# Kernel tuning notes

Hardware: AMD Instinct MI355X
Metric: run time of the kernel (lower is better)

## Reference

```python
import jax, jax.numpy as jnp
import numpy as np

MODEL_DIM = 1024
N_HEADS = 16
HEAD_DIM = 64  # q_dim == k_dim == v_dim


def setup_inputs() -> dict:
    key = jax.random.key(0)
    ks = jax.random.split(key, 7)
    B, S = 4, 2048
    scale = 1.0 / np.sqrt(MODEL_DIM)
    return {
        "q": jax.random.normal(ks[0], (B, S, MODEL_DIM), dtype=jnp.float32),
        "k": jax.random.normal(ks[1], (B, S, MODEL_DIM), dtype=jnp.float32),
        "v": jax.random.normal(ks[2], (B, S, MODEL_DIM), dtype=jnp.float32),
        # Linear weights stored as [out, in] like torch; no biases.
        "wq": jax.random.normal(ks[3], (N_HEADS * HEAD_DIM, MODEL_DIM), dtype=jnp.float32) * scale,
        "wk": jax.random.normal(ks[4], (N_HEADS * HEAD_DIM, MODEL_DIM), dtype=jnp.float32) * scale,
        "wv": jax.random.normal(ks[5], (N_HEADS * HEAD_DIM, MODEL_DIM), dtype=jnp.float32) * scale,
        "wo": jax.random.normal(ks[6], (MODEL_DIM, N_HEADS * HEAD_DIM), dtype=jnp.float32) * scale,
    }


def reference(q, k, v, wq, wk, wv, wo):
    B, Sq, _ = q.shape
    Sk = k.shape[1]
    # projections: [B,S,D] @ W^T -> [B,S,H*dh] -> [B,H,S,dh]
    qh = (q @ wq.T).reshape(B, Sq, N_HEADS, HEAD_DIM).transpose(0, 2, 1, 3)
    kh = (k @ wk.T).reshape(B, Sk, N_HEADS, HEAD_DIM).transpose(0, 2, 1, 3)
    vh = (v @ wv.T).reshape(B, Sk, N_HEADS, HEAD_DIM).transpose(0, 2, 1, 3)
    # scores [B,H,Sq,Sk], scaled by sqrt(k_dim)
    scores = jnp.einsum('bhqd,bhkd->bhqk', qh, kh) / jnp.sqrt(jnp.float32(HEAD_DIM))
    attn = jax.nn.softmax(scores, axis=-1)
    ctx = jnp.einsum('bhqk,bhkd->bhqd', attn, vh)  # [B,H,Sq,dh]
    ctx = ctx.transpose(0, 2, 1, 3).reshape(B, Sq, N_HEADS * HEAD_DIM)
    return ctx @ wo.T
```

## Files before the change

### kernel.cpp

```cpp
#include <hip/hip_runtime.h>
#include <cstdint>
#include <cstddef>


typedef _Float16 f16x8 __attribute__((ext_vector_type(8)));
typedef _Float16 f16x4 __attribute__((ext_vector_type(4)));
typedef _Float16 f16x2 __attribute__((ext_vector_type(2)));
typedef __fp16 h16x2 __attribute__((ext_vector_type(2)));
typedef float f32x4 __attribute__((ext_vector_type(4)));
typedef float f32x16 __attribute__((ext_vector_type(16)));
typedef unsigned u32x4 __attribute__((ext_vector_type(4)));
typedef int i32x2 __attribute__((ext_vector_type(2)));

#define LDS_CAST(p) ((__attribute__((address_space(3))) void*)(p))
#define GLB_CAST(p) ((const __attribute__((address_space(1))) void*)(p))

__device__ __forceinline__ void gload_lds16(const void* g, void* l) {
  __builtin_amdgcn_global_load_lds(GLB_CAST(g), LDS_CAST(l), 16, 0, 0);
}

__device__ __forceinline__ float fexp2(float x) {
#if __has_builtin(__builtin_amdgcn_exp2f)
  return __builtin_amdgcn_exp2f(x);
#else
  return exp2f(x);
#endif
}

__device__ __forceinline__ f16x2 pkrtz(float a, float b) {
  h16x2 r = __builtin_amdgcn_cvt_pkrtz(a, b);
  return __builtin_bit_cast(f16x2, r);
}

__device__ __forceinline__ float dot2acc(f16x2 a, float acc) {
#if __has_builtin(__builtin_amdgcn_fdot2)
  const f16x2 one2 = {(_Float16)1.0f, (_Float16)1.0f};
  return __builtin_amdgcn_fdot2(a, one2, acc, false);
#else
  return acc + (float)a[0] + (float)a[1];
#endif
}

__device__ __forceinline__ void pl32swap(unsigned& a, unsigned& b) {
#if __has_builtin(__builtin_amdgcn_permlane32_swap)
  i32x2 r = __builtin_amdgcn_permlane32_swap((int)a, (int)b, false, false);
  a = (unsigned)r[0];
  b = (unsigned)r[1];
#else
  asm("v_permlane32_swap_b32 %0, %1" : "+v"(a), "+v"(b));
#endif
}

__global__ void cvt_all(const float* __restrict__ q, const float* __restrict__ k,
                        const float* __restrict__ v, const float* __restrict__ wq,
                        const float* __restrict__ wk, const float* __restrict__ wv,
                        const float* __restrict__ wo, _Float16* __restrict__ oq,
                        _Float16* __restrict__ ok, _Float16* __restrict__ ov,
                        _Float16* __restrict__ owq, _Float16* __restrict__ owk,
                        _Float16* __restrict__ owv, _Float16* __restrict__ owo) {
  int id = blockIdx.x;
  const float* in;
  _Float16* out;
  int base;
  if (id < 24576) {
    int z = id >> 13;
    base = (id & 8191) * 256;
    in = z == 0 ? q : z == 1 ? k : v;
    out = z == 0 ? oq : z == 1 ? ok : ov;
  } else {
    int id2 = id - 24576;
    int z = id2 >> 10;
    base = (id2 & 1023) * 256;
    in = z == 0 ? wq : z == 1 ? wk : z == 2 ? wv : wo;
    out = z == 0 ? owq : z == 1 ? owk : z == 2 ? owv : owo;
  }
  int i = base + threadIdx.x;
  float4 vv = ((const float4*)in)[i];
  f16x4 o = {(_Float16)vv.x, (_Float16)vv.y, (_Float16)vv.z, (_Float16)vv.w};
  ((f16x4*)out)[i] = o;
}

template <int MODE>
__device__ __forceinline__ void gemm_core(const _Float16* __restrict__ A,
                                          const _Float16* __restrict__ W,
                                          void* __restrict__ C, float scale,
                                          _Float16* As, _Float16* Bs) {
  constexpr int K = 1024, N = 1024;
  const int tid = threadIdx.x;
  const int wid = tid >> 6;
  const int lane = tid & 63;
  const int quad = lane >> 4;
  const int l16 = lane & 15;
  const int wm = wid >> 1;
  const int wn = wid & 1;

  int lin = blockIdx.y * 8 + blockIdx.x;
  int swz = (lin & 7) * 64 + (lin >> 3);
  const int m0 = (swz >> 3) * 128;
  const int n0 = (swz & 7) * 128;

  const _Float16* Ag = A + (size_t)m0 * K;
  const _Float16* Bg = W + (size_t)n0 * K;

  f32x4 acc[4][4];
#pragma unroll
  for (int i = 0; i < 4; i++)
#pragma unroll
    for (int j = 0; j < 4; j++) acc[i][j] = (f32x4){0.f, 0.f, 0.f, 0.f};

  const int lrow = lane >> 2;
  const int swsrc = ((lane & 3) ^ ((lane >> 3) & 3)) * 8;

  auto stage = [&](_Float16* Ad, _Float16* Bd, int k0) {
#pragma unroll
    for (int i = 0; i < 2; i++) {
      int issue = wid * 2 + i;
      gload_lds16(Ag + (size_t)(issue * 16 + lrow) * K + k0 + swsrc,
                  Ad + issue * 512);
      gload_lds16(Bg + (size_t)(issue * 16 + lrow) * K + k0 + swsrc,
                  Bd + issue * 512);
    }
  };

  const int swq = (quad ^ ((l16 >> 1) & 3)) * 8;

  auto compute = [&](const _Float16* Ab, const _Float16* Bb) {
    f16x8 af[4], bfr[4];
#pragma unroll
    for (int mt = 0; mt < 4; mt++)
      af[mt] = *(const f16x8*)&Ab[(wm * 64 + mt * 16 + l16) * 32 + swq];
#pragma unroll
    for (int nt = 0; nt < 4; nt++)
      bfr[nt] = *(const f16x8*)&Bb[(wn * 64 + nt * 16 + l16) * 32 + swq];
#pragma unroll
    for (int mt = 0; mt < 4; mt++)
#pragma unroll
      for (int nt = 0; nt < 4; nt++)
        acc[mt][nt] = __builtin_amdgcn_mfma_f32_16x16x32_f16(
            af[mt], bfr[nt], acc[mt][nt], 0, 0, 0);
  };

  _Float16* A0 = As;
  _Float16* A1 = As + 4096;
  _Float16* B0 = Bs;
  _Float16* B1 = Bs + 4096;

  stage(A0, B0, 0);
  asm volatile("s_waitcnt vmcnt(0)" ::: "memory");
  __builtin_amdgcn_s_barrier();

  for (int g = 0; g < 15; g++) {
    int t2 = g * 2;
    stage(A1, B1, (t2 + 1) * 32);
    compute(A0, B0);
    asm volatile("s_waitcnt vmcnt(0)" ::: "memory");
    __builtin_amdgcn_s_barrier();
    stage(A0, B0, (t2 + 2) * 32);
    compute(A1, B1);
    asm volatile("s_waitcnt vmcnt(0)" ::: "memory");
    __builtin_amdgcn_s_barrier();
  }
  stage(A1, B1, 31 * 32);
  compute(A0, B0);
  asm volatile("s_waitcnt vmcnt(0)" ::: "memory");
  __builtin_amdgcn_s_barrier();
  compute(A1, B1);

#pragma unroll
  for (int mt = 0; mt < 4; mt++) {
#pragma unroll
    for (int nt = 0; nt < 4; nt++) {
#pragma unroll
      for (int r = 0; r < 4; r++) {
        int m = m0 + wm * 64 + mt * 16 + quad * 4 + r;
        int n = n0 + wn * 64 + nt * 16 + l16;
        float v = acc[mt][nt][r] * scale;
        if (MODE == 0) {
          ((float*)C)[(size_t)m * N + n] = v;
        } else {
          int b = m >> 11, s = m & 2047;
          int h = n >> 6, dd = n & 63;
          size_t bh = (size_t)(b * 16 + h);
          if (MODE == 1) {
            ((_Float16*)C)[(bh * 2048 + s) * 64 + dd] = (_Float16)v;
          } else if (MODE == 3) {
            int kt2 = s >> 5, l32k = s & 31;
            int s4 = dd >> 4, hi8 = (dd >> 3) & 1, j = dd & 7;
            size_t idx = (bh * 32 + (kt2 >> 1)) * 8192 +
                         (((kt2 & 1) * 4 + s4) * 512) + (hi8 * 32 + l32k) * 8 +
                         j;
            ((_Float16*)C)[idx] = (_Float16)v;
          } else {
            int kt = s >> 6, ks = (s >> 4) & 3, hi8 = (s >> 3) & 1, j = s & 7;
            int dt = dd >> 5, l32v = dd & 31;
            size_t idx = (bh * 32 + kt) * 8192 + 4096 + ((dt * 4 + ks) * 512) +
                         (hi8 * 32 + l32v) * 8 + j;
            ((_Float16*)C)[idx] = (_Float16)v;
          }
        }
      }
    }
  }
}

__global__ __launch_bounds__(256, 4) void gemm_qkv(
    const _Float16* __restrict__ qb, const _Float16* __restrict__ kb,
    const _Float16* __restrict__ vb, const _Float16* __restrict__ wq,
    const _Float16* __restrict__ wk, const _Float16* __restrict__ wv,
    _Float16* __restrict__ Qh, _Float16* __restrict__ KVf) {
  __shared__ _Float16 As[2 * 128 * 32];
  __shared__ _Float16 Bs[2 * 128 * 32];
  if (blockIdx.z == 0)
    gemm_core<1>(qb, wq, Qh, 0.18033688f, As, Bs);
  else if (blockIdx.z == 1)
    gemm_core<3>(kb, wk, KVf, 1.0f, As, Bs);
  else
    gemm_core<4>(vb, wv, KVf, 1.0f, As, Bs);
}

__global__ __launch_bounds__(256, 4) void gemm_wo(
    const _Float16* __restrict__ ctx, const _Float16* __restrict__ wo,
    float* __restrict__ out) {
  __shared__ _Float16 As[2 * 128 * 32];
  __shared__ _Float16 Bs[2 * 128 * 32];
  gemm_core<0>(ctx, wo, out, 1.0f, As, Bs);
}

__global__ __launch_bounds__(256, 3) void attn_kernel(
    const _Float16* __restrict__ Qh, const _Float16* __restrict__ KVf,
    _Float16* __restrict__ ctx) {
  __shared__ _Float16 sKV[3][8192];

  const int id = blockIdx.x;
  const int xcd = id & 7;
  const int sub = id >> 3;
  const int bh = xcd * 8 + (sub >> 4);
  const int qt = sub & 15;
  const int tid = threadIdx.x;
  const int wid = tid >> 6;
  const int lane = tid & 63;
  const int l32 = lane & 31;
  const int hi = lane >> 5;

  const _Float16* Qg = Qh + ((size_t)bh * 2048 + qt * 128 + wid * 32) * 64;
  const _Float16* KVb = KVf + (size_t)bh * 262144;

  f16x8 aq[4];
#pragma unroll
  for (int s = 0; s < 4; s++)
    aq[s] = *(const f16x8*)(Qg + (size_t)l32 * 64 + s * 16 + hi * 8);

  f32x16 acc[2];
#pragma unroll
  for (int i = 0; i < 16; i++) {
    acc[0][i] = 0.f;
    acc[1][i] = 0.f;
  }
  float lsA = 0.f, lsB = 0.f;

  auto stage = [&](int buf, int kt) {
    const _Float16* t = KVb + (size_t)kt * 8192;
#pragma unroll
    for (int i = 0; i < 4; i++) {
      int c = wid * 4 + i;
      gload_lds16(t + c * 512 + lane * 8, &sKV[buf][c * 512]);
    }
  };

  auto body = [&](const _Float16* Ks) {
    const _Float16* Vs = Ks + 4096;
#pragma unroll
    for (int st = 0; st < 2; st++) {
      f16x8 kf[4];
#pragma unroll
      for (int s = 0; s < 4; s++)
        kf[s] = *(const f16x8*)&Ks[(st * 4 + s) * 512 + lane * 8];

      f32x16 sacc;
#pragma unroll
      for (int i = 0; i < 16; i++) sacc[i] = 0.f;
#pragma unroll
      for (int s = 0; s < 4; s++)
        sacc =
            __builtin_amdgcn_mfma_f32_32x32x16_f16(kf[s], aq[s], sacc, 0, 0, 0);

      f16x8 vta[2], vtb[2];
#pragma unroll
      for (int kh = 0; kh < 2; kh++) {
        int g = st * 2 + kh;
        vta[kh] = *(const f16x8*)&Vs[g * 512 + lane * 8];
        vtb[kh] = *(const f16x8*)&Vs[(4 + g) * 512 + lane * 8];
      }

      unsigned hw[8];
#pragma unroll
      for (int i = 0; i < 8; i++) {
        f16x2 hh = pkrtz(fexp2(sacc[2 * i]), fexp2(sacc[2 * i + 1]));
        if (i & 1)
          lsB = dot2acc(hh, lsB);
        else
          lsA = dot2acc(hh, lsA);
        hw[i] = __builtin_bit_cast(unsigned, hh);
      }

#pragma unroll
      for (int kh = 0; kh < 2; kh++) {
        unsigned w0 = hw[4 * kh + 0], w2 = hw[4 * kh + 2];
        unsigned w1 = hw[4 * kh + 1], w3 = hw[4 * kh + 3];
        pl32swap(w0, w2);
        pl32swap(w1, w3);
        u32x4 wv4 = {w0, w1, w2, w3};
        f16x8 pfrag = __builtin_bit_cast(f16x8, wv4);
        acc[0] = __builtin_amdgcn_mfma_f32_32x32x16_f16(vta[kh], pfrag, acc[0],
                                                        0, 0, 0);
        acc[1] = __builtin_amdgcn_mfma_f32_32x32x16_f16(vtb[kh], pfrag, acc[1],
                                                        0, 0, 0);
      }
    }
  };

  stage(0, 0);
  for (int g = 0; g < 10; g++) {
    int t3 = g * 3;
    stage(1, t3 + 1);
    asm volatile("s_waitcnt vmcnt(4)" ::: "memory");
    __builtin_amdgcn_s_barrier();
    asm volatile("" ::: "memory");
    body(sKV[0]);
    stage(2, t3 + 2);
    asm volatile("s_waitcnt vmcnt(4)" ::: "memory");
    __builtin_amdgcn_s_barrier();
    asm volatile("" ::: "memory");
    body(sKV[1]);
    stage(0, t3 + 3);
    asm volatile("s_waitcnt vmcnt(4)" ::: "memory");
    __builtin_amdgcn_s_barrier();
    asm volatile("" ::: "memory");
    body(sKV[2]);
  }
  stage(1, 31);
  asm volatile("s_waitcnt vmcnt(4)" ::: "memory");
  __builtin_amdgcn_s_barrier();
  asm volatile("" ::: "memory");
  body(sKV[0]);
  asm volatile("s_waitcnt vmcnt(0)" ::: "memory");
  __builtin_amdgcn_s_barrier();
  asm volatile("" ::: "memory");
  body(sKV[1]);

  float lsum = lsA + lsB;
  float l = lsum + __shfl_xor(lsum, 32);
  float inv = 1.f / l;
  const int b = bh >> 4, h = bh & 15;
  int q = qt * 128 + wid * 32 + l32;
  _Float16* outp = ctx + ((size_t)b * 2048 + q) * 1024 + h * 64;
#pragma unroll
  for (int dt = 0; dt < 2; dt++)
#pragma unroll
    for (int g = 0; g < 4; g++) {
      f16x4 o;
#pragma unroll
      for (int c = 0; c < 4; c++) o[c] = (_Float16)(acc[dt][g * 4 + c] * inv);
      *(f16x4*)(outp + dt * 32 + g * 8 + hi * 4) = o;
    }
}

extern "C" void kernel_launch(void* const* d_in, const int* in_sizes, int n_in,
                              void* d_out, int out_size, void* d_ws,
                              size_t ws_size, hipStream_t stream) {
  const float* q = (const float*)d_in[0];
  const float* k = (const float*)d_in[1];
  const float* v = (const float*)d_in[2];
  const float* wq = (const float*)d_in[3];
  const float* wk = (const float*)d_in[4];
  const float* wv = (const float*)d_in[5];
  const float* wo = (const float*)d_in[6];
  float* out = (float*)d_out;

  const size_t SD = (size_t)8192 * 1024;
  const size_t WSZ = (size_t)1024 * 1024;

  _Float16* ws = (_Float16*)d_ws;
  _Float16* qb = ws;
  _Float16* kb = ws + 1 * SD;
  _Float16* vb = ws + 2 * SD;
  _Float16* Qh = ws + 3 * SD;
  _Float16* KVf = ws + 4 * SD;
  _Float16* ctx = ws + 6 * SD;
  _Float16* wqb = ws + 7 * SD;
  _Float16* wkb = wqb + WSZ;
  _Float16* wvb = wqb + 2 * WSZ;
  _Float16* wob = wqb + 3 * WSZ;

  cvt_all<<<dim3(28672), 256, 0, stream>>>(q, k, v, wq, wk, wv, wo, qb, kb, vb,
                                           wqb, wkb, wvb, wob);

  gemm_qkv<<<dim3(8, 64, 3), 256, 0, stream>>>(qb, kb, vb, wqb, wkb, wvb, Qh,
                                               KVf);

  attn_kernel<<<dim3(1024), 256, 0, stream>>>(Qh, KVf, ctx);

  gemm_wo<<<dim3(8, 64), 256, 0, stream>>>(ctx, wob, out);
}
```

Baseline: 332.4 us.

## Fuse fp32-to-fp16 activation conversion into QKV projection GEMM loads

Removes the separate pass that converts q, k and v from fp32 to fp16. The QKV GEMM now stages fp32 activation tiles straight into LDS with an XOR swizzle and converts them to fp16 when forming MFMA fragments. Only the weights are still converted in a small pre-kernel. This saves a full read-write round trip over about 100MB of activations. In exchange the A tile uses twice the LDS, occupancy bounds drop from 4 to 3 blocks, the per-tile global reads double, and conversion instructions are added to the inner loop, where each A element is converted once per N-tile.

```diff
diff --git a/kernel.cpp b/kernel.cpp
--- a/kernel.cpp
+++ b/kernel.cpp
@@ -51,40 +51,25 @@
 #endif
 }
 
-__global__ void cvt_all(const float* __restrict__ q, const float* __restrict__ k,
-                        const float* __restrict__ v, const float* __restrict__ wq,
-                        const float* __restrict__ wk, const float* __restrict__ wv,
-                        const float* __restrict__ wo, _Float16* __restrict__ oq,
-                        _Float16* __restrict__ ok, _Float16* __restrict__ ov,
-                        _Float16* __restrict__ owq, _Float16* __restrict__ owk,
-                        _Float16* __restrict__ owv, _Float16* __restrict__ owo) {
+__global__ void cvt_w(const float* __restrict__ wq, const float* __restrict__ wk,
+                      const float* __restrict__ wv, const float* __restrict__ wo,
+                      _Float16* __restrict__ owq, _Float16* __restrict__ owk,
+                      _Float16* __restrict__ owv, _Float16* __restrict__ owo) {
   int id = blockIdx.x;
-  const float* in;
-  _Float16* out;
-  int base;
-  if (id < 24576) {
-    int z = id >> 13;
-    base = (id & 8191) * 256;
-    in = z == 0 ? q : z == 1 ? k : v;
-    out = z == 0 ? oq : z == 1 ? ok : ov;
-  } else {
-    int id2 = id - 24576;
-    int z = id2 >> 10;
-    base = (id2 & 1023) * 256;
-    in = z == 0 ? wq : z == 1 ? wk : z == 2 ? wv : wo;
-    out = z == 0 ? owq : z == 1 ? owk : z == 2 ? owv : owo;
-  }
-  int i = base + threadIdx.x;
-  float4 vv = ((const float4*)in)[i];
-  f16x4 o = {(_Float16)vv.x, (_Float16)vv.y, (_Float16)vv.z, (_Float16)vv.w};
+  int z = id >> 10;
+  const float* in = z == 0 ? wq : z == 1 ? wk : z == 2 ? wv : wo;
+  _Float16* out = z == 0 ? owq : z == 1 ? owk : z == 2 ? owv : owo;
+  int i = (id & 1023) * 256 + threadIdx.x;
+  float4 v = ((const float4*)in)[i];
+  f16x4 o = {(_Float16)v.x, (_Float16)v.y, (_Float16)v.z, (_Float16)v.w};
   ((f16x4*)out)[i] = o;
 }
 
-template <int MODE>
-__device__ __forceinline__ void gemm_core(const _Float16* __restrict__ A,
+template <int MODE, bool AF32>
+__device__ __forceinline__ void gemm_core(const void* __restrict__ Aptr,
                                           const _Float16* __restrict__ W,
                                           void* __restrict__ C, float scale,
-                                          _Float16* As, _Float16* Bs) {
+                                          void* AsRaw, _Float16* Bs) {
   constexpr int K = 1024, N = 1024;
   const int tid = threadIdx.x;
   const int wid = tid >> 6;
@@ -99,8 +84,11 @@
   const int m0 = (swz >> 3) * 128;
   const int n0 = (swz & 7) * 128;
 
-  const _Float16* Ag = A + (size_t)m0 * K;
+  const float* Ag32 = (const float*)Aptr + (size_t)m0 * K;
+  const _Float16* Ag16 = (const _Float16*)Aptr + (size_t)m0 * K;
   const _Float16* Bg = W + (size_t)n0 * K;
+  float* As32 = (float*)AsRaw;
+  _Float16* As16 = (_Float16*)AsRaw;
 
   f32x4 acc[4][4];
 #pragma unroll
@@ -111,24 +99,57 @@
   const int lrow = lane >> 2;
   const int swsrc = ((lane & 3) ^ ((lane >> 3) & 3)) * 8;
 
-  auto stage = [&](_Float16* Ad, _Float16* Bd, int k0) {
+  auto stageAB16 = [&](_Float16* Ad, _Float16* Bd, int k0) {
 #pragma unroll
     for (int i = 0; i < 2; i++) {
       int issue = wid * 2 + i;
-      gload_lds16(Ag + (size_t)(issue * 16 + lrow) * K + k0 + swsrc,
+      gload_lds16(Ag16 + (size_t)(issue * 16 + lrow) * K + k0 + swsrc,
                   Ad + issue * 512);
       gload_lds16(Bg + (size_t)(issue * 16 + lrow) * K + k0 + swsrc,
                   Bd + issue * 512);
     }
   };
+  auto stageB = [&](_Float16* Bd, int k0) {
+#pragma unroll
+    for (int i = 0; i < 2; i++) {
+      int issue = wid * 2 + i;
+      gload_lds16(Bg + (size_t)(issue * 16 + lrow) * K + k0 + swsrc,
+                  Bd + issue * 512);
+    }
+  };
+  const int a32row = lane >> 3;
+  const int a32sl = ((lane & 7) ^ (lane >> 3)) * 4;
+  auto stageA32 = [&](float* Ad, int k0) {
+#pragma unroll
+    for (int i = 0; i < 4; i++) {
+      int c = wid * 4 + i;
+      gload_lds16(Ag32 + (size_t)(c * 8 + a32row) * K + k0 + a32sl,
+                  Ad + c * 256);
+    }
+  };
 
   const int swq = (quad ^ ((l16 >> 1) & 3)) * 8;
-
-  auto compute = [&](const _Float16* Ab, const _Float16* Bb) {
+  const int ax = l16 & 7;
+
+  auto compute = [&](const void* Ab, const _Float16* Bb) {
     f16x8 af[4], bfr[4];
-#pragma unroll
-    for (int mt = 0; mt < 4; mt++)
-      af[mt] = *(const f16x8*)&Ab[(wm * 64 + mt * 16 + l16) * 32 + swq];
+    if constexpr (AF32) {
+      const float* A32 = (const float*)Ab;
+#pragma unroll
+      for (int mt = 0; mt < 4; mt++) {
+        int row = wm * 64 + mt * 16 + l16;
+        f32x4 a0 = *(const f32x4*)&A32[row * 32 + (((2 * quad) ^ ax) * 4)];
+        f32x4 a1 = *(const f32x4*)&A32[row * 32 + (((2 * quad + 1) ^ ax) * 4)];
+        af[mt] = (f16x8){(_Float16)a0[0], (_Float16)a0[1], (_Float16)a0[2],
+                         (_Float16)a0[3], (_Float16)a1[0], (_Float16)a1[1],
+                         (_Float16)a1[2], (_Float16)a1[3]};
+      }
+    } else {
+      const _Float16* A16 = (const _Float16*)Ab;
+#pragma unroll
+      for (int mt = 0; mt < 4; mt++)
+        af[mt] = *(const f16x8*)&A16[(wm * 64 + mt * 16 + l16) * 32 + swq];
+    }
 #pragma unroll
     for (int nt = 0; nt < 4; nt++)
       bfr[nt] = *(const f16x8*)&Bb[(wn * 64 + nt * 16 + l16) * 32 + swq];
@@ -140,31 +161,58 @@
             af[mt], bfr[nt], acc[mt][nt], 0, 0, 0);
   };
 
-  _Float16* A0 = As;
-  _Float16* A1 = As + 4096;
   _Float16* B0 = Bs;
   _Float16* B1 = Bs + 4096;
 
-  stage(A0, B0, 0);
-  asm volatile("s_waitcnt vmcnt(0)" ::: "memory");
-  __builtin_amdgcn_s_barrier();
-
-  for (int g = 0; g < 15; g++) {
-    int t2 = g * 2;
-    stage(A1, B1, (t2 + 1) * 32);
+  if constexpr (AF32) {
+    float* A0 = As32;
+    float* A1 = As32 + 4096;
+    stageA32(A0, 0);
+    stageB(B0, 0);
+    asm volatile("s_waitcnt vmcnt(0)" ::: "memory");
+    __builtin_amdgcn_s_barrier();
+    for (int g = 0; g < 15; g++) {
+      int t2 = g * 2;
+      stageA32(A1, (t2 + 1) * 32);
+      stageB(B1, (t2 + 1) * 32);
+      compute(A0, B0);
+      asm volatile("s_waitcnt vmcnt(0)" ::: "memory");
+      __builtin_amdgcn_s_barrier();
+      stageA32(A0, (t2 + 2) * 32);
+      stageB(B0, (t2 + 2) * 32);
+      compute(A1, B1);
+      asm volatile("s_waitcnt vmcnt(0)" ::: "memory");
+      __builtin_amdgcn_s_barrier();
+    }
+    stageA32(A1, 31 * 32);
+    stageB(B1, 31 * 32);
     compute(A0, B0);
     asm volatile("s_waitcnt vmcnt(0)" ::: "memory");
     __builtin_amdgcn_s_barrier();
-    stage(A0, B0, (t2 + 2) * 32);
     compute(A1, B1);
+  } else {
+    _Float16* A0 = As16;
+    _Float16* A1 = As16 + 4096;
+    stageAB16(A0, B0, 0);
     asm volatile("s_waitcnt vmcnt(0)" ::: "memory");
     __builtin_amdgcn_s_barrier();
+    for (int g = 0; g < 15; g++) {
+      int t2 = g * 2;
+      stageAB16(A1, B1, (t2 + 1) * 32);
+      compute(A0, B0);
+      asm volatile("s_waitcnt vmcnt(0)" ::: "memory");
+      __builtin_amdgcn_s_barrier();
+      stageAB16(A0, B0, (t2 + 2) * 32);
+      compute(A1, B1);
+      asm volatile("s_waitcnt vmcnt(0)" ::: "memory");
+      __builtin_amdgcn_s_barrier();
+    }
+    stageAB16(A1, B1, 31 * 32);
+    compute(A0, B0);
+    asm volatile("s_waitcnt vmcnt(0)" ::: "memory");
+    __builtin_amdgcn_s_barrier();
+    compute(A1, B1);
   }
-  stage(A1, B1, 31 * 32);
-  compute(A0, B0);
-  asm volatile("s_waitcnt vmcnt(0)" ::: "memory");
-  __builtin_amdgcn_s_barrier();
-  compute(A1, B1);
 
 #pragma unroll
   for (int mt = 0; mt < 4; mt++) {
@@ -203,19 +251,19 @@
   }
 }
 
-__global__ __launch_bounds__(256, 4) void gemm_qkv(
-    const _Float16* __restrict__ qb, const _Float16* __restrict__ kb,
-    const _Float16* __restrict__ vb, const _Float16* __restrict__ wq,
+__global__ __launch_bounds__(256, 3) void gemm_qkv(
+    const float* __restrict__ q, const float* __restrict__ k,
+    const float* __restrict__ v, const _Float16* __restrict__ wq,
     const _Float16* __restrict__ wk, const _Float16* __restrict__ wv,
     _Float16* __restrict__ Qh, _Float16* __restrict__ KVf) {
-  __shared__ _Float16 As[2 * 128 * 32];
-  __shared__ _Float16 Bs[2 * 128 * 32];
+  __shared__ float As32[2 * 4096];
+  __shared__ _Float16 Bs[2 * 4096];
   if (blockIdx.z == 0)
-    gemm_core<1>(qb, wq, Qh, 0.18033688f, As, Bs);
+    gemm_core<1, true>(q, wq, Qh, 0.18033688f, As32, Bs);
   else if (blockIdx.z == 1)
-    gemm_core<3>(kb, wk, KVf, 1.0f, As, Bs);
+    gemm_core<3, true>(k, wk, KVf, 1.0f, As32, Bs);
   else
-    gemm_core<4>(vb, wv, KVf, 1.0f, As, Bs);
+    gemm_core<4, true>(v, wv, KVf, 1.0f, As32, Bs);
 }
 
 __global__ __launch_bounds__(256, 4) void gemm_wo(
@@ -223,7 +271,7 @@
     float* __restrict__ out) {
   __shared__ _Float16 As[2 * 128 * 32];
   __shared__ _Float16 Bs[2 * 128 * 32];
-  gemm_core<0>(ctx, wo, out, 1.0f, As, Bs);
+  gemm_core<0, false>(ctx, wo, out, 1.0f, As, Bs);
 }
 
 __global__ __launch_bounds__(256, 3) void attn_kernel(
@@ -381,9 +429,6 @@
   const size_t WSZ = (size_t)1024 * 1024;
 
   _Float16* ws = (_Float16*)d_ws;
-  _Float16* qb = ws;
-  _Float16* kb = ws + 1 * SD;
-  _Float16* vb = ws + 2 * SD;
   _Float16* Qh = ws + 3 * SD;
   _Float16* KVf = ws + 4 * SD;
   _Float16* ctx = ws + 6 * SD;
@@ -392,10 +437,9 @@
   _Float16* wvb = wqb + 2 * WSZ;
   _Float16* wob = wqb + 3 * WSZ;
 
-  cvt_all<<<dim3(28672), 256, 0, stream>>>(q, k, v, wq, wk, wv, wo, qb, kb, vb,
-                                           wqb, wkb, wvb, wob);
-
-  gemm_qkv<<<dim3(8, 64, 3), 256, 0, stream>>>(qb, kb, vb, wqb, wkb, wvb, Qh,
+  cvt_w<<<dim3(4096), 256, 0, stream>>>(wq, wk, wv, wo, wqb, wkb, wvb, wob);
+
+  gemm_qkv<<<dim3(8, 64, 3), 256, 0, stream>>>(q, k, v, wqb, wkb, wvb, Qh,
                                                KVf);
 
   attn_kernel<<<dim3(1024), 256, 0, stream>>>(Qh, KVf, ctx);
```

After: 344.0 us. +3.5%, slower.
